# Kernel optimization log

Measured on AMD Instinct MI355X. Metric: run time of the kernel, lower is better.

The kernel has to match this reference:

```python
import jax, jax.numpy as jnp
import numpy as np

N = 50000
E = 800000
IN_C = 128
HID = 128
EMB = 128
OUT_C = 40
BN_EPS = 1e-5


def setup_inputs() -> dict:
    key = jax.random.key(0)
    ks = jax.random.split(key, 24)
    inp = {}
    inp['x'] = jax.random.normal(ks[0], (N, IN_C), dtype=jnp.float32)
    inp['edge_index'] = jax.random.randint(ks[1], (2, E), 0, N, dtype=jnp.int32)
    # GCNConv weights (PyG GCNConv: out = norm_agg(x @ W) + b)
    dims = [(IN_C, HID), (HID, HID), (HID, HID + EMB)]
    for i, (fi, fo) in enumerate(dims, 1):
        inp[f'conv_w{i}'] = jax.random.normal(ks[2 * i], (fi, fo), dtype=jnp.float32) / np.sqrt(fi)
        inp[f'conv_b{i}'] = jnp.zeros((fo,), dtype=jnp.float32)
        # BatchNorm (eval mode: running stats)
        inp[f'bn_g{i}'] = jax.random.uniform(ks[2 * i + 1], (fo,), minval=0.5, maxval=1.5, dtype=jnp.float32)
        inp[f'bn_b{i}'] = jax.random.normal(jax.random.fold_in(ks[2 * i + 1], 1), (fo,), dtype=jnp.float32) * 0.1
        inp[f'bn_m{i}'] = jax.random.normal(jax.random.fold_in(ks[2 * i + 1], 2), (fo,), dtype=jnp.float32) * 0.1
        inp[f'bn_v{i}'] = jax.random.uniform(jax.random.fold_in(ks[2 * i + 1], 3), (fo,), minval=0.5, maxval=1.5, dtype=jnp.float32)
    inp['lin_w1'] = jax.random.normal(ks[20], (HID + EMB, HID), dtype=jnp.float32) / np.sqrt(HID + EMB)
    inp['lin_b1'] = jnp.zeros((HID,), dtype=jnp.float32)
    inp['lin_w2'] = jax.random.normal(ks[21], (HID, OUT_C), dtype=jnp.float32) / np.sqrt(HID)
    inp['lin_b2'] = jnp.zeros((OUT_C,), dtype=jnp.float32)
    return inp


def _gcn_norm(edge_index, n):
    # add self-loops, symmetric normalization D^-1/2 (A+I) D^-1/2
    loops = jnp.arange(n, dtype=edge_index.dtype)
    src = jnp.concatenate([edge_index[0], loops])
    dst = jnp.concatenate([edge_index[1], loops])
    deg = jax.ops.segment_sum(jnp.ones_like(dst, dtype=jnp.float32), dst, num_segments=n)
    dinv = jax.lax.rsqrt(jnp.maximum(deg, 1.0))
    norm = dinv[src] * dinv[dst]
    return src, dst, norm


def _gcn_layer(x, w, b, src, dst, norm, n):
    xw = x @ w                      # [N, Fo] dense GEMM
    msg = xw[src] * norm[:, None]   # [E+N, Fo] gather + scale
    out = jax.ops.segment_sum(msg, dst, num_segments=n)  # scatter-add
    return out + b


def _bn_eval(h, g, b, m, v):
    return (h - m) * jax.lax.rsqrt(v + BN_EPS) * g + b


def reference(x, edge_index,
              conv_w1, conv_b1, bn_g1, bn_b1, bn_m1, bn_v1,
              conv_w2, conv_b2, bn_g2, bn_b2, bn_m2, bn_v2,
              conv_w3, conv_b3, bn_g3, bn_b3, bn_m3, bn_v3,
              lin_w1, lin_b1, lin_w2, lin_b2):
    n = x.shape[0]
    src, dst, norm = _gcn_norm(edge_index, n)
    convs = [(conv_w1, conv_b1, bn_g1, bn_b1, bn_m1, bn_v1),
             (conv_w2, conv_b2, bn_g2, bn_b2, bn_m2, bn_v2),
             (conv_w3, conv_b3, bn_g3, bn_b3, bn_m3, bn_v3)]
    h = x
    for (w, b, g, bb, m, v) in convs:
        h = _gcn_layer(h, w, b, src, dst, norm, n)
        h = jax.nn.relu(_bn_eval(h, g, bb, m, v))
        # dropout: identity (eval mode)
    h = jax.nn.relu(h @ lin_w1 + lin_b1)
    return h @ lin_w2 + lin_b2
```

## Files before the change

kernel.cpp:

```cpp
#include <hip/hip_runtime.h>
#include <hip/hip_fp16.h>


typedef _Float16 f16x8 __attribute__((ext_vector_type(8)));
typedef float f32x4 __attribute__((ext_vector_type(4)));

static inline int cdiv(int a, int b) { return (a + b - 1) / b; }

__global__ __launch_bounds__(256) void k_zero_int(int* p, int n) {
    int i = blockIdx.x * 256 + threadIdx.x;
    if (i < n) p[i] = 0;
}

__global__ __launch_bounds__(256) void k_bcount(const int* __restrict__ ei, int E,
                                                int* bucketCount, int* blockBase) {
    __shared__ int lh[256];
    lh[threadIdx.x] = 0;
    __syncthreads();
    int base = blockIdx.x * 2048;
#pragma unroll
    for (int i = 0; i < 8; ++i) {
        int e = base + i * 256 + threadIdx.x;
        if (e < E) atomicAdd(&lh[ei[E + e] >> 8], 1);
    }
    __syncthreads();
    blockBase[blockIdx.x * 256 + threadIdx.x] =
        atomicAdd(&bucketCount[threadIdx.x], lh[threadIdx.x]);
}

__global__ void k_bscan(const int* __restrict__ bucketCount, int* bucketPtr, int nbk,
                        int* rowptr, int N, int E) {
    __shared__ int s[1024];
    int v = (threadIdx.x < nbk) ? bucketCount[threadIdx.x] : 0;
    s[threadIdx.x] = v;
    __syncthreads();
    for (int off = 1; off < 1024; off <<= 1) {
        int t = (threadIdx.x >= (unsigned)off) ? s[threadIdx.x - off] : 0;
        __syncthreads();
        s[threadIdx.x] += t;
        __syncthreads();
    }
    if (threadIdx.x < nbk) bucketPtr[threadIdx.x] = s[threadIdx.x] - v;
    if (threadIdx.x == 0) {
        bucketPtr[nbk] = E;
        rowptr[N] = E;
    }
}

__global__ __launch_bounds__(256) void k_bscatter(const int* __restrict__ ei, int E,
                                                  const int* __restrict__ bucketPtr,
                                                  const int* __restrict__ blockBase,
                                                  int2* __restrict__ ebuf) {
    __shared__ int lh[256];
    lh[threadIdx.x] = 0;
    __syncthreads();
    int base = blockIdx.x * 2048;
    const int* bb = &blockBase[blockIdx.x * 256];
#pragma unroll
    for (int i = 0; i < 8; ++i) {
        int e = base + i * 256 + threadIdx.x;
        if (e < E) {
            int src = ei[e];
            int dst = ei[E + e];
            int b = dst >> 8;
            int lp = atomicAdd(&lh[b], 1);
            ebuf[bucketPtr[b] + bb[b] + lp] = int2{src, dst};
        }
    }
}

__global__ __launch_bounds__(256) void k_bcsr(const int2* __restrict__ ebuf,
                                              const int* __restrict__ bucketPtr,
                                              int* __restrict__ rowptr, float* __restrict__ dinv,
                                              int* __restrict__ csr, int N) {
    __shared__ int hist[256], excl[256], cur[256];
    const int b = blockIdx.x;
    const int base = bucketPtr[b];
    const int cnt = bucketPtr[b + 1] - base;
    const int t = threadIdx.x;
    hist[t] = 0;
    cur[t] = 0;
    __syncthreads();
    for (int i = t; i < cnt; i += 256) atomicAdd(&hist[ebuf[base + i].y & 255], 1);
    __syncthreads();
    int v = hist[t];
    excl[t] = v;
    __syncthreads();
    for (int off = 1; off < 256; off <<= 1) {
        int x = (t >= off) ? excl[t - off] : 0;
        __syncthreads();
        excl[t] += x;
        __syncthreads();
    }
    int ex = excl[t] - v;
    int node = b * 256 + t;
    if (node < N) {
        rowptr[node] = base + ex;
        dinv[node] = rsqrtf((float)(v + 1));
    }
    __syncthreads();
    excl[t] = ex;
    __syncthreads();
    for (int i = t; i < cnt; i += 256) {
        int2 e = ebuf[base + i];
        int ln = e.y & 255;
        int pos = base + excl[ln] + atomicAdd(&cur[ln], 1);
        csr[pos] = e.x;
    }
}

__global__ __launch_bounds__(256) void k_f2h(const float* __restrict__ x, __half* __restrict__ y,
                                             int n4) {
    int i = blockIdx.x * 256 + threadIdx.x;
    if (i >= n4) return;
    float4 v = ((const float4*)x)[i];
    __half h[4] = {__float2half_rn(v.x), __float2half_rn(v.y), __float2half_rn(v.z),
                   __float2half_rn(v.w)};
    ((uint2*)y)[i] = *(uint2*)h;
}

__device__ inline bool wt_job(int i, int lo, int hi, int K, int FO, const float* W, __half* T) {
    if (i < lo || i >= hi) return false;
    int j = i - lo;
    int c = j / K;
    int k = j - c * K;
    T[j] = (c < FO) ? __float2half_rn(W[(size_t)k * FO + c]) : __half(0.f);
    return true;
}

__global__ __launch_bounds__(256) void k_wt_all(const float* w1, const float* w2, const float* w3,
                                                const float* w4, const float* w5, __half* t1,
                                                __half* t2, __half* t3, __half* t4, __half* t5) {
    int i = blockIdx.x * 256 + threadIdx.x;
    if (wt_job(i, 0, 16384, 128, 128, w1, t1)) return;
    if (wt_job(i, 16384, 32768, 128, 128, w2, t2)) return;
    if (wt_job(i, 32768, 65536, 128, 256, w3, t3)) return;
    if (wt_job(i, 65536, 98304, 256, 128, w4, t4)) return;
    wt_job(i, 98304, 106496, 128, 40, w5, t5);
}

__global__ __launch_bounds__(256) void k_gather64(const int* __restrict__ rowptr,
                                                  const int* __restrict__ csr,
                                                  const float* __restrict__ dinv,
                                                  const __half* __restrict__ xh,
                                                  __half* __restrict__ G, int N) {
    int t = blockIdx.x * 256 + threadIdx.x;
    int node = t >> 6;
    if (node >= N) return;
    int lane = t & 63;
    const __half2* xb = (const __half2*)xh;
    float di = dinv[node];
    float ax, ay;
    {
        float2 f = __half22float2(xb[(size_t)node * 64 + lane]);
        float s = di * di;
        ax = s * f.x;
        ay = s * f.y;
    }
    int p0 = rowptr[node], p1 = rowptr[node + 1];
    int p = p0;
    for (; p + 8 <= p1; p += 8) {
        int s_[8];
        float wg[8];
        __half2 v[8];
#pragma unroll
        for (int j = 0; j < 8; ++j) s_[j] = csr[p + j];
#pragma unroll
        for (int j = 0; j < 8; ++j) wg[j] = di * dinv[s_[j]];
#pragma unroll
        for (int j = 0; j < 8; ++j) v[j] = xb[(size_t)s_[j] * 64 + lane];
#pragma unroll
        for (int j = 0; j < 8; ++j) {
            float2 f = __half22float2(v[j]);
            ax += wg[j] * f.x;
            ay += wg[j] * f.y;
        }
    }
    for (; p + 4 <= p1; p += 4) {
        int s_[4];
        float wg[4];
        __half2 v[4];
#pragma unroll
        for (int j = 0; j < 4; ++j) s_[j] = csr[p + j];
#pragma unroll
        for (int j = 0; j < 4; ++j) wg[j] = di * dinv[s_[j]];
#pragma unroll
        for (int j = 0; j < 4; ++j) v[j] = xb[(size_t)s_[j] * 64 + lane];
#pragma unroll
        for (int j = 0; j < 4; ++j) {
            float2 f = __half22float2(v[j]);
            ax += wg[j] * f.x;
            ay += wg[j] * f.y;
        }
    }
    for (; p < p1; ++p) {
        int src = csr[p];
        float w = di * dinv[src];
        float2 f = __half22float2(xb[(size_t)src * 64 + lane]);
        ax += w * f.x;
        ay += w * f.y;
    }
    ((__half2*)G)[(size_t)node * 64 + lane] = __floats2half2_rn(ax, ay);
}

template <int K, bool BN, bool RELU, typename OT>
__global__ __launch_bounds__(256) void k_mfma(const __half* __restrict__ A,
                                              const __half* __restrict__ Wt,
                                              const float* __restrict__ cb,
                                              const float* __restrict__ g,
                                              const float* __restrict__ bb,
                                              const float* __restrict__ m,
                                              const float* __restrict__ vv,
                                              OT* __restrict__ Y, int ldy, int N, int ncols) {
    constexpr int KS = K / 32;
    constexpr int NCT = 4;
    __shared__ __half bs[KS * NCT * 64 * 8];

    const int tid = threadIdx.x;
    const int col0 = blockIdx.y * 64;

    constexpr int PIECES = KS * NCT * 64;
#pragma unroll
    for (int p = tid; p < PIECES; p += 256) {
        int ks = p / (NCT * 64);
        int rem = p - ks * (NCT * 64);
        int ct = rem >> 6;
        int l = rem & 63;
        int col = col0 + ct * 16 + (l & 15);
        int kg = ks * 32 + (l >> 4) * 8;
        *(uint4*)&bs[p * 8] = *(const uint4*)&Wt[(size_t)col * K + kg];
    }
    __syncthreads();

    const int wave = tid >> 6;
    const int lane = tid & 63;
    const int rbase = blockIdx.x * 128 + wave * 32;
    const int r0 = rbase + (lane & 15);
    const int k0 = (lane >> 4) * 8;

    uint4 af[2][KS];
#pragma unroll
    for (int ks = 0; ks < KS; ++ks) {
        int kk = ks * 32 + k0;
        af[0][ks] = (r0 < N) ? *(const uint4*)&A[(size_t)r0 * K + kk] : uint4{0, 0, 0, 0};
        af[1][ks] = (r0 + 16 < N) ? *(const uint4*)&A[(size_t)(r0 + 16) * K + kk]
                                  : uint4{0, 0, 0, 0};
    }

    f32x4 acc[2][NCT];
#pragma unroll
    for (int rt = 0; rt < 2; ++rt)
#pragma unroll
        for (int ct = 0; ct < NCT; ++ct) acc[rt][ct] = {0.f, 0.f, 0.f, 0.f};

#pragma unroll
    for (int ks = 0; ks < KS; ++ks) {
        f16x8 b[NCT];
#pragma unroll
        for (int ct = 0; ct < NCT; ++ct)
            b[ct] = *(const f16x8*)&bs[((ks * NCT + ct) * 64 + lane) * 8];
#pragma unroll
        for (int rt = 0; rt < 2; ++rt) {
            f16x8 a = *(const f16x8*)&af[rt][ks];
#pragma unroll
            for (int ct = 0; ct < NCT; ++ct)
                acc[rt][ct] = __builtin_amdgcn_mfma_f32_16x16x32_f16(a, b[ct], acc[rt][ct], 0, 0, 0);
        }
    }

    const int cbase = col0 + (lane & 15);
#pragma unroll
    for (int ct = 0; ct < NCT; ++ct) {
        int col = cbase + ct * 16;
        if (col >= ncols) continue;
        float sc, sh;
        if (BN) {
            sc = g[col] * rsqrtf(vv[col] + 1e-5f);
            sh = bb[col] + (cb[col] - m[col]) * sc;
        } else {
            sc = 1.f;
            sh = cb[col];
        }
#pragma unroll
        for (int rt = 0; rt < 2; ++rt) {
#pragma unroll
            for (int r = 0; r < 4; ++r) {
                int row = rbase + rt * 16 + (lane >> 4) * 4 + r;
                if (row < N) {
                    float o = acc[rt][ct][r] * sc + sh;
                    if (RELU) o = fmaxf(o, 0.f);
                    if constexpr (sizeof(OT) == 2) {
                        Y[(size_t)row * ldy + col] = __float2half_rn(o);
                    } else {
                        Y[(size_t)row * ldy + col] = o;
                    }
                }
            }
        }
    }
}

extern "C" void kernel_launch(void* const* d_in, const int* in_sizes, int n_in,
                              void* d_out, int out_size, void* d_ws, size_t ws_size,
                              hipStream_t stream) {
    const float* x = (const float*)d_in[0];
    const int* ei = (const int*)d_in[1];
    const float* cw1 = (const float*)d_in[2];
    const float* cb1 = (const float*)d_in[3];
    const float* g1 = (const float*)d_in[4];
    const float* bb1 = (const float*)d_in[5];
    const float* m1 = (const float*)d_in[6];
    const float* v1 = (const float*)d_in[7];
    const float* cw2 = (const float*)d_in[8];
    const float* cb2 = (const float*)d_in[9];
    const float* g2 = (const float*)d_in[10];
    const float* bb2 = (const float*)d_in[11];
    const float* m2 = (const float*)d_in[12];
    const float* v2 = (const float*)d_in[13];
    const float* cw3 = (const float*)d_in[14];
    const float* cb3 = (const float*)d_in[15];
    const float* g3 = (const float*)d_in[16];
    const float* bb3 = (const float*)d_in[17];
    const float* m3 = (const float*)d_in[18];
    const float* v3 = (const float*)d_in[19];
    const float* lw1 = (const float*)d_in[20];
    const float* lb1 = (const float*)d_in[21];
    const float* lw2 = (const float*)d_in[22];
    const float* lb2 = (const float*)d_in[23];
    float* out = (float*)d_out;

    const int N = in_sizes[0] / 128;
    const int E = in_sizes[1] / 2;
    const int NBK = cdiv(N, 256);
    const int NBA = cdiv(E, 2048);

    auto al = [](size_t v) { return (v + 255) & ~(size_t)255; };
    char* w = (char*)d_ws;
    size_t o = 0;
    float* dinv  = (float*)(w + o);  o = al(o + (size_t)N * 4);
    int* rowptr  = (int*)(w + o);    o = al(o + (size_t)(N + 1) * 4);
    int* bcount  = (int*)(w + o);    o = al(o + 256 * 4);
    int* bptr    = (int*)(w + o);    o = al(o + (256 + 1) * 4);
    int* bbase   = (int*)(w + o);    o = al(o + (size_t)NBA * 256 * 4);
    int2* ebuf   = (int2*)(w + o);   o = al(o + (size_t)E * 8);
    int* csr     = (int*)(w + o);    o = al(o + (size_t)E * 4);
    __half* XH   = (__half*)(w + o); o = al(o + (size_t)N * 128 * 2);
    __half* GH   = (__half*)(w + o); o = al(o + (size_t)N * 128 * 2);
    __half* H3h  = (__half*)(w + o); o = al(o + (size_t)N * 256 * 2);
    __half* Wt1  = (__half*)(w + o); o = al(o + (size_t)128 * 128 * 2);
    __half* Wt2  = (__half*)(w + o); o = al(o + (size_t)128 * 128 * 2);
    __half* Wt3  = (__half*)(w + o); o = al(o + (size_t)256 * 128 * 2);
    __half* Wt4  = (__half*)(w + o); o = al(o + (size_t)128 * 256 * 2);
    __half* Wt5  = (__half*)(w + o); o = al(o + (size_t)64 * 128 * 2);
    __half* Zh   = GH;

    k_zero_int<<<1, 256, 0, stream>>>(bcount, 256);
    k_bcount<<<NBA, 256, 0, stream>>>(ei, E, bcount, bbase);
    k_bscan<<<1, 1024, 0, stream>>>(bcount, bptr, NBK, rowptr, N, E);
    k_bscatter<<<NBA, 256, 0, stream>>>(ei, E, bptr, bbase, ebuf);
    k_bcsr<<<NBK, 256, 0, stream>>>(ebuf, bptr, rowptr, dinv, csr, N);

    k_f2h<<<cdiv(N * 32, 256), 256, 0, stream>>>(x, XH, N * 32);
    k_wt_all<<<cdiv(106496, 256), 256, 0, stream>>>(cw1, cw2, cw3, lw1, lw2, Wt1, Wt2, Wt3, Wt4,
                                                    Wt5);

    const int gx = cdiv(N, 128);

    k_gather64<<<cdiv(N, 4), 256, 0, stream>>>(rowptr, csr, dinv, XH, GH, N);
    k_mfma<128, true, true, __half><<<dim3(gx, 2), 256, 0, stream>>>(
        GH, Wt1, cb1, g1, bb1, m1, v1, XH, 128, N, 128);
    k_gather64<<<cdiv(N, 4), 256, 0, stream>>>(rowptr, csr, dinv, XH, GH, N);
    k_mfma<128, true, true, __half><<<dim3(gx, 2), 256, 0, stream>>>(
        GH, Wt2, cb2, g2, bb2, m2, v2, XH, 128, N, 128);
    k_gather64<<<cdiv(N, 4), 256, 0, stream>>>(rowptr, csr, dinv, XH, GH, N);
    k_mfma<128, true, true, __half><<<dim3(gx, 4), 256, 0, stream>>>(
        GH, Wt3, cb3, g3, bb3, m3, v3, H3h, 256, N, 256);
    k_mfma<256, false, true, __half><<<dim3(gx, 2), 256, 0, stream>>>(
        H3h, Wt4, lb1, nullptr, nullptr, nullptr, nullptr, Zh, 128, N, 128);
    k_mfma<128, false, false, float><<<dim3(gx, 1), 256, 0, stream>>>(
        Zh, Wt5, lb2, nullptr, nullptr, nullptr, nullptr, out, 40, N, 40);
}
```

Baseline: 223.5 us.

## Split node features into 32-column slices for cache-resident gathers

Node features are now stored in a slice-major blocked layout of four 32-column slices, each N×32 halves. The gather kernel processes one slice at a time, so the randomly accessed working set per pass is about a quarter of the full feature matrix and fits better in L2/MALL. Within each wavefront, four groups of 16 lanes each handle a different edge, and the partial sums are combined with cross-lane shuffles. The conv GEMMs write their outputs in the blocked layout. The cost is 64-byte random row reads instead of 256-byte ones, four times as many blocks, and the CSR indices being re-read once per slice.

```diff
diff --git a/kernel.cpp b/kernel.cpp
--- a/kernel.cpp
+++ b/kernel.cpp
@@ -109,14 +109,18 @@
     }
 }
 
-__global__ __launch_bounds__(256) void k_f2h(const float* __restrict__ x, __half* __restrict__ y,
-                                             int n4) {
+__global__ __launch_bounds__(256) void k_f2h_blk(const float* __restrict__ x,
+                                                 __half* __restrict__ XB, int N) {
     int i = blockIdx.x * 256 + threadIdx.x;
-    if (i >= n4) return;
-    float4 v = ((const float4*)x)[i];
+    if (i >= N * 32) return;
+    int r = i >> 5;
+    int q = i & 31;
+    float4 v = *(const float4*)&x[(size_t)r * 128 + q * 4];
     __half h[4] = {__float2half_rn(v.x), __float2half_rn(v.y), __float2half_rn(v.z),
                    __float2half_rn(v.w)};
-    ((uint2*)y)[i] = *(uint2*)h;
+    int b = q >> 3;
+    int co = (q * 4) & 31;
+    *(uint2*)&XB[((size_t)b * N + r) * 32 + co] = *(uint2*)h;
 }
 
 __device__ inline bool wt_job(int i, int lo, int hi, int K, int FO, const float* W, __half* T) {
@@ -139,71 +143,63 @@
     wt_job(i, 98304, 106496, 128, 40, w5, t5);
 }
 
-__global__ __launch_bounds__(256) void k_gather64(const int* __restrict__ rowptr,
-                                                  const int* __restrict__ csr,
-                                                  const float* __restrict__ dinv,
-                                                  const __half* __restrict__ xh,
-                                                  __half* __restrict__ G, int N) {
-    int t = blockIdx.x * 256 + threadIdx.x;
-    int node = t >> 6;
+__global__ __launch_bounds__(256) void k_gather_slice(const int* __restrict__ rowptr,
+                                                      const int* __restrict__ csr,
+                                                      const float* __restrict__ dinv,
+                                                      const __half* __restrict__ XB,
+                                                      __half* __restrict__ G, int N, int BPS) {
+    int blk = blockIdx.x;
+    int s = blk / BPS;
+    int nb = blk - s * BPS;
+    int node = nb * 4 + (threadIdx.x >> 6);
     if (node >= N) return;
-    int lane = t & 63;
-    const __half2* xb = (const __half2*)xh;
+    int lane = threadIdx.x & 63;
+    int eg = lane >> 4;
+    int c = lane & 15;
+    const __half2* xs = (const __half2*)(XB + (size_t)s * N * 32);
     float di = dinv[node];
-    float ax, ay;
-    {
-        float2 f = __half22float2(xb[(size_t)node * 64 + lane]);
-        float s = di * di;
-        ax = s * f.x;
-        ay = s * f.y;
-    }
     int p0 = rowptr[node], p1 = rowptr[node + 1];
+    float ax = 0.f, ay = 0.f;
     int p = p0;
     for (; p + 8 <= p1; p += 8) {
-        int s_[8];
-        float wg[8];
-        __half2 v[8];
-#pragma unroll
-        for (int j = 0; j < 8; ++j) s_[j] = csr[p + j];
-#pragma unroll
-        for (int j = 0; j < 8; ++j) wg[j] = di * dinv[s_[j]];
-#pragma unroll
-        for (int j = 0; j < 8; ++j) v[j] = xb[(size_t)s_[j] * 64 + lane];
-#pragma unroll
-        for (int j = 0; j < 8; ++j) {
-            float2 f = __half22float2(v[j]);
-            ax += wg[j] * f.x;
-            ay += wg[j] * f.y;
-        }
-    }
-    for (; p + 4 <= p1; p += 4) {
-        int s_[4];
-        float wg[4];
-        __half2 v[4];
-#pragma unroll
-        for (int j = 0; j < 4; ++j) s_[j] = csr[p + j];
-#pragma unroll
-        for (int j = 0; j < 4; ++j) wg[j] = di * dinv[s_[j]];
-#pragma unroll
-        for (int j = 0; j < 4; ++j) v[j] = xb[(size_t)s_[j] * 64 + lane];
-#pragma unroll
-        for (int j = 0; j < 4; ++j) {
-            float2 f = __half22float2(v[j]);
-            ax += wg[j] * f.x;
-            ay += wg[j] * f.y;
-        }
-    }
-    for (; p < p1; ++p) {
-        int src = csr[p];
-        float w = di * dinv[src];
-        float2 f = __half22float2(xb[(size_t)src * 64 + lane]);
-        ax += w * f.x;
-        ay += w * f.y;
-    }
-    ((__half2*)G)[(size_t)node * 64 + lane] = __floats2half2_rn(ax, ay);
-}
-
-template <int K, bool BN, bool RELU, typename OT>
+        int sA = csr[p + eg], sB = csr[p + 4 + eg];
+        float wA = di * dinv[sA], wB = di * dinv[sB];
+        float2 fA = __half22float2(xs[(size_t)sA * 16 + c]);
+        float2 fB = __half22float2(xs[(size_t)sB * 16 + c]);
+        ax += wA * fA.x + wB * fB.x;
+        ay += wA * fA.y + wB * fB.y;
+    }
+    if (p + 4 <= p1) {
+        int sA = csr[p + eg];
+        float wA = di * dinv[sA];
+        float2 fA = __half22float2(xs[(size_t)sA * 16 + c]);
+        ax += wA * fA.x;
+        ay += wA * fA.y;
+        p += 4;
+    }
+    if (p + eg < p1) {
+        int sA = csr[p + eg];
+        float wA = di * dinv[sA];
+        float2 fA = __half22float2(xs[(size_t)sA * 16 + c]);
+        ax += wA * fA.x;
+        ay += wA * fA.y;
+    }
+    ax += __shfl_xor(ax, 16, 64);
+    ay += __shfl_xor(ay, 16, 64);
+    ax += __shfl_xor(ax, 32, 64);
+    ay += __shfl_xor(ay, 32, 64);
+    if (eg == 0) {
+        float sdi = di * di;
+        float2 f = __half22float2(xs[(size_t)node * 16 + c]);
+        ax += sdi * f.x;
+        ay += sdi * f.y;
+        __half2 hv = __floats2half2_rn(ax, ay);
+        __builtin_nontemporal_store(*(unsigned int*)&hv,
+                                    (unsigned int*)&G[(size_t)node * 128 + s * 32 + c * 2]);
+    }
+}
+
+template <int K, bool BN, bool RELU, bool BLKOUT, typename OT>
 __global__ __launch_bounds__(256) void k_mfma(const __half* __restrict__ A,
                                               const __half* __restrict__ Wt,
                                               const float* __restrict__ cb,
@@ -289,7 +285,10 @@
                 if (row < N) {
                     float o = acc[rt][ct][r] * sc + sh;
                     if (RELU) o = fmaxf(o, 0.f);
-                    if constexpr (sizeof(OT) == 2) {
+                    if constexpr (BLKOUT) {
+                        ((__half*)Y)[((size_t)(col >> 5) * ldy + row) * 32 + (col & 31)] =
+                            __float2half_rn(o);
+                    } else if constexpr (sizeof(OT) == 2) {
                         Y[(size_t)row * ldy + col] = __float2half_rn(o);
                     } else {
                         Y[(size_t)row * ldy + col] = o;
@@ -333,6 +332,7 @@
     const int E = in_sizes[1] / 2;
     const int NBK = cdiv(N, 256);
     const int NBA = cdiv(E, 2048);
+    const int BPS = cdiv(N, 4);
 
     auto al = [](size_t v) { return (v + 255) & ~(size_t)255; };
     char* w = (char*)d_ws;
@@ -344,7 +344,7 @@
     int* bbase   = (int*)(w + o);    o = al(o + (size_t)NBA * 256 * 4);
     int2* ebuf   = (int2*)(w + o);   o = al(o + (size_t)E * 8);
     int* csr     = (int*)(w + o);    o = al(o + (size_t)E * 4);
-    __half* XH   = (__half*)(w + o); o = al(o + (size_t)N * 128 * 2);
+    __half* XB   = (__half*)(w + o); o = al(o + (size_t)N * 128 * 2);
     __half* GH   = (__half*)(w + o); o = al(o + (size_t)N * 128 * 2);
     __half* H3h  = (__half*)(w + o); o = al(o + (size_t)N * 256 * 2);
     __half* Wt1  = (__half*)(w + o); o = al(o + (size_t)128 * 128 * 2);
@@ -360,23 +360,23 @@
     k_bscatter<<<NBA, 256, 0, stream>>>(ei, E, bptr, bbase, ebuf);
     k_bcsr<<<NBK, 256, 0, stream>>>(ebuf, bptr, rowptr, dinv, csr, N);
 
-    k_f2h<<<cdiv(N * 32, 256), 256, 0, stream>>>(x, XH, N * 32);
+    k_f2h_blk<<<cdiv(N * 32, 256), 256, 0, stream>>>(x, XB, N);
     k_wt_all<<<cdiv(106496, 256), 256, 0, stream>>>(cw1, cw2, cw3, lw1, lw2, Wt1, Wt2, Wt3, Wt4,
                                                     Wt5);
 
     const int gx = cdiv(N, 128);
 
-    k_gather64<<<cdiv(N, 4), 256, 0, stream>>>(rowptr, csr, dinv, XH, GH, N);
-    k_mfma<128, true, true, __half><<<dim3(gx, 2), 256, 0, stream>>>(
-        GH, Wt1, cb1, g1, bb1, m1, v1, XH, 128, N, 128);
-    k_gather64<<<cdiv(N, 4), 256, 0, stream>>>(rowptr, csr, dinv, XH, GH, N);
-    k_mfma<128, true, true, __half><<<dim3(gx, 2), 256, 0, stream>>>(
-        GH, Wt2, cb2, g2, bb2, m2, v2, XH, 128, N, 128);
-    k_gather64<<<cdiv(N, 4), 256, 0, stream>>>(rowptr, csr, dinv, XH, GH, N);
-    k_mfma<128, true, true, __half><<<dim3(gx, 4), 256, 0, stream>>>(
+    k_gather_slice<<<4 * BPS, 256, 0, stream>>>(rowptr, csr, dinv, XB, GH, N, BPS);
+    k_mfma<128, true, true, true, __half><<<dim3(gx, 2), 256, 0, stream>>>(
+        GH, Wt1, cb1, g1, bb1, m1, v1, XB, N, N, 128);
+    k_gather_slice<<<4 * BPS, 256, 0, stream>>>(rowptr, csr, dinv, XB, GH, N, BPS);
+    k_mfma<128, true, true, true, __half><<<dim3(gx, 2), 256, 0, stream>>>(
+        GH, Wt2, cb2, g2, bb2, m2, v2, XB, N, N, 128);
+    k_gather_slice<<<4 * BPS, 256, 0, stream>>>(rowptr, csr, dinv, XB, GH, N, BPS);
+    k_mfma<128, true, true, false, __half><<<dim3(gx, 4), 256, 0, stream>>>(
         GH, Wt3, cb3, g3, bb3, m3, v3, H3h, 256, N, 256);
-    k_mfma<256, false, true, __half><<<dim3(gx, 2), 256, 0, stream>>>(
+    k_mfma<256, false, true, false, __half><<<dim3(gx, 2), 256, 0, stream>>>(
         H3h, Wt4, lb1, nullptr, nullptr, nullptr, nullptr, Zh, 128, N, 128);
-    k_mfma<128, false, false, float><<<dim3(gx, 1), 256, 0, stream>>>(
+    k_mfma<128, false, false, false, float><<<dim3(gx, 1), 256, 0, stream>>>(
         Zh, Wt5, lb2, nullptr, nullptr, nullptr, nullptr, out, 40, N, 40);
 }
```

Result: slower. 363.8 us (+62.8%).

## Split gather into column halves with two-way edge parallelism per wavefront

Applied to the files above, without the earlier changes.

The gather kernel now covers each node with two blocks, one per 64-column half of the feature row. Within a wavefront the two 32-lane halves process alternate edges and combine their partial sums with a cross-lane shuffle. This is meant to raise memory-level parallelism and occupancy for low-degree nodes, at the cost of reading the CSR indices and dinv values twice and doing 128-byte rather than 256-byte row segment loads. The fp32-to-fp16 feature conversion and the weight transpose kernels are also merged into one launch.

```diff
diff --git a/kernel.cpp b/kernel.cpp
--- a/kernel.cpp
+++ b/kernel.cpp
@@ -109,16 +109,6 @@
     }
 }
 
-__global__ __launch_bounds__(256) void k_f2h(const float* __restrict__ x, __half* __restrict__ y,
-                                             int n4) {
-    int i = blockIdx.x * 256 + threadIdx.x;
-    if (i >= n4) return;
-    float4 v = ((const float4*)x)[i];
-    __half h[4] = {__float2half_rn(v.x), __float2half_rn(v.y), __float2half_rn(v.z),
-                   __float2half_rn(v.w)};
-    ((uint2*)y)[i] = *(uint2*)h;
-}
-
 __device__ inline bool wt_job(int i, int lo, int hi, int K, int FO, const float* W, __half* T) {
     if (i < lo || i >= hi) return false;
     int j = i - lo;
@@ -128,47 +118,56 @@
     return true;
 }
 
-__global__ __launch_bounds__(256) void k_wt_all(const float* w1, const float* w2, const float* w3,
-                                                const float* w4, const float* w5, __half* t1,
-                                                __half* t2, __half* t3, __half* t4, __half* t5) {
+__global__ __launch_bounds__(256) void k_prep(const float* __restrict__ x, __half* __restrict__ XH,
+                                              int nf,
+                                              const float* w1, const float* w2, const float* w3,
+                                              const float* w4, const float* w5, __half* t1,
+                                              __half* t2, __half* t3, __half* t4, __half* t5) {
     int i = blockIdx.x * 256 + threadIdx.x;
-    if (wt_job(i, 0, 16384, 128, 128, w1, t1)) return;
-    if (wt_job(i, 16384, 32768, 128, 128, w2, t2)) return;
-    if (wt_job(i, 32768, 65536, 128, 256, w3, t3)) return;
-    if (wt_job(i, 65536, 98304, 256, 128, w4, t4)) return;
-    wt_job(i, 98304, 106496, 128, 40, w5, t5);
-}
-
-__global__ __launch_bounds__(256) void k_gather64(const int* __restrict__ rowptr,
-                                                  const int* __restrict__ csr,
-                                                  const float* __restrict__ dinv,
-                                                  const __half* __restrict__ xh,
-                                                  __half* __restrict__ G, int N) {
-    int t = blockIdx.x * 256 + threadIdx.x;
-    int node = t >> 6;
+    if (i < nf) {
+        float4 v = ((const float4*)x)[i];
+        __half h[4] = {__float2half_rn(v.x), __float2half_rn(v.y), __float2half_rn(v.z),
+                       __float2half_rn(v.w)};
+        ((uint2*)XH)[i] = *(uint2*)h;
+        return;
+    }
+    int j = i - nf;
+    if (wt_job(j, 0, 16384, 128, 128, w1, t1)) return;
+    if (wt_job(j, 16384, 32768, 128, 128, w2, t2)) return;
+    if (wt_job(j, 32768, 65536, 128, 256, w3, t3)) return;
+    if (wt_job(j, 65536, 98304, 256, 128, w4, t4)) return;
+    wt_job(j, 98304, 106496, 128, 40, w5, t5);
+}
+
+__global__ __launch_bounds__(256) void k_gather2(const int* __restrict__ rowptr,
+                                                 const int* __restrict__ csr,
+                                                 const float* __restrict__ dinv,
+                                                 const __half* __restrict__ xh,
+                                                 __half* __restrict__ G, int N, int BPS) {
+    int blk = blockIdx.x;
+    int s = blk / BPS;
+    int nb = blk - s * BPS;
+    int node = nb * 4 + (threadIdx.x >> 6);
     if (node >= N) return;
-    int lane = t & 63;
-    const __half2* xb = (const __half2*)xh;
+    int lane = threadIdx.x & 63;
+    int half = lane >> 5;
+    int c = lane & 31;
+    const __half2* xs = (const __half2*)xh;
+    const int cofs = s * 32 + c;
     float di = dinv[node];
-    float ax, ay;
-    {
-        float2 f = __half22float2(xb[(size_t)node * 64 + lane]);
-        float s = di * di;
-        ax = s * f.x;
-        ay = s * f.y;
-    }
     int p0 = rowptr[node], p1 = rowptr[node + 1];
+    float ax = 0.f, ay = 0.f;
     int p = p0;
-    for (; p + 8 <= p1; p += 8) {
+    for (; p + 16 <= p1; p += 16) {
         int s_[8];
         float wg[8];
         __half2 v[8];
 #pragma unroll
-        for (int j = 0; j < 8; ++j) s_[j] = csr[p + j];
+        for (int j = 0; j < 8; ++j) s_[j] = csr[p + 2 * j + half];
 #pragma unroll
         for (int j = 0; j < 8; ++j) wg[j] = di * dinv[s_[j]];
 #pragma unroll
-        for (int j = 0; j < 8; ++j) v[j] = xb[(size_t)s_[j] * 64 + lane];
+        for (int j = 0; j < 8; ++j) v[j] = xs[(size_t)s_[j] * 64 + cofs];
 #pragma unroll
         for (int j = 0; j < 8; ++j) {
             float2 f = __half22float2(v[j]);
@@ -176,31 +175,29 @@
             ay += wg[j] * f.y;
         }
     }
-    for (; p + 4 <= p1; p += 4) {
-        int s_[4];
-        float wg[4];
-        __half2 v[4];
-#pragma unroll
-        for (int j = 0; j < 4; ++j) s_[j] = csr[p + j];
-#pragma unroll
-        for (int j = 0; j < 4; ++j) wg[j] = di * dinv[s_[j]];
-#pragma unroll
-        for (int j = 0; j < 4; ++j) v[j] = xb[(size_t)s_[j] * 64 + lane];
-#pragma unroll
-        for (int j = 0; j < 4; ++j) {
-            float2 f = __half22float2(v[j]);
-            ax += wg[j] * f.x;
-            ay += wg[j] * f.y;
-        }
-    }
-    for (; p < p1; ++p) {
-        int src = csr[p];
-        float w = di * dinv[src];
-        float2 f = __half22float2(xb[(size_t)src * 64 + lane]);
-        ax += w * f.x;
-        ay += w * f.y;
-    }
-    ((__half2*)G)[(size_t)node * 64 + lane] = __floats2half2_rn(ax, ay);
+    for (; p + 2 <= p1; p += 2) {
+        int sA = csr[p + half];
+        float wA = di * dinv[sA];
+        float2 f = __half22float2(xs[(size_t)sA * 64 + cofs]);
+        ax += wA * f.x;
+        ay += wA * f.y;
+    }
+    if (p < p1) {
+        int sA = csr[p1 - 1];
+        float wA = half ? 0.f : di * dinv[sA];
+        float2 f = __half22float2(xs[(size_t)sA * 64 + cofs]);
+        ax += wA * f.x;
+        ay += wA * f.y;
+    }
+    ax += __shfl_xor(ax, 32, 64);
+    ay += __shfl_xor(ay, 32, 64);
+    if (half == 0) {
+        float sdi = di * di;
+        float2 f = __half22float2(xs[(size_t)node * 64 + cofs]);
+        ax += sdi * f.x;
+        ay += sdi * f.y;
+        ((__half2*)G)[(size_t)node * 64 + cofs] = __floats2half2_rn(ax, ay);
+    }
 }
 
 template <int K, bool BN, bool RELU, typename OT>
@@ -333,6 +330,7 @@
     const int E = in_sizes[1] / 2;
     const int NBK = cdiv(N, 256);
     const int NBA = cdiv(E, 2048);
+    const int BPS = cdiv(N, 4);
 
     auto al = [](size_t v) { return (v + 255) & ~(size_t)255; };
     char* w = (char*)d_ws;
@@ -360,19 +358,18 @@
     k_bscatter<<<NBA, 256, 0, stream>>>(ei, E, bptr, bbase, ebuf);
     k_bcsr<<<NBK, 256, 0, stream>>>(ebuf, bptr, rowptr, dinv, csr, N);
 
-    k_f2h<<<cdiv(N * 32, 256), 256, 0, stream>>>(x, XH, N * 32);
-    k_wt_all<<<cdiv(106496, 256), 256, 0, stream>>>(cw1, cw2, cw3, lw1, lw2, Wt1, Wt2, Wt3, Wt4,
-                                                    Wt5);
+    k_prep<<<cdiv(N * 32 + 106496, 256), 256, 0, stream>>>(x, XH, N * 32, cw1, cw2, cw3, lw1,
+                                                           lw2, Wt1, Wt2, Wt3, Wt4, Wt5);
 
     const int gx = cdiv(N, 128);
 
-    k_gather64<<<cdiv(N, 4), 256, 0, stream>>>(rowptr, csr, dinv, XH, GH, N);
+    k_gather2<<<2 * BPS, 256, 0, stream>>>(rowptr, csr, dinv, XH, GH, N, BPS);
     k_mfma<128, true, true, __half><<<dim3(gx, 2), 256, 0, stream>>>(
         GH, Wt1, cb1, g1, bb1, m1, v1, XH, 128, N, 128);
-    k_gather64<<<cdiv(N, 4), 256, 0, stream>>>(rowptr, csr, dinv, XH, GH, N);
+    k_gather2<<<2 * BPS, 256, 0, stream>>>(rowptr, csr, dinv, XH, GH, N, BPS);
     k_mfma<128, true, true, __half><<<dim3(gx, 2), 256, 0, stream>>>(
         GH, Wt2, cb2, g2, bb2, m2, v2, XH, 128, N, 128);
-    k_gather64<<<cdiv(N, 4), 256, 0, stream>>>(rowptr, csr, dinv, XH, GH, N);
+    k_gather2<<<2 * BPS, 256, 0, stream>>>(rowptr, csr, dinv, XH, GH, N, BPS);
     k_mfma<128, true, true, __half><<<dim3(gx, 4), 256, 0, stream>>>(
         GH, Wt3, cb3, g3, bb3, m3, v3, H3h, 256, N, 256);
     k_mfma<256, false, true, __half><<<dim3(gx, 2), 256, 0, stream>>>(
```

Result: slower. 314.9 us (+40.9%).
